# Kernel tuning notes

Hardware: AMD Instinct MI355X
Metric: run time of the kernel (lower is better)

Reference implementation:

```python
import jax, jax.numpy as jnp
import numpy as np

N_NODES = 100000
N_EDGES = 1600000
IN_CH = 128
HID = 64
N_CLASSES = 16
N_GRAPHS = 64


def setup_inputs() -> dict:
    key = jax.random.key(0)
    ks = jax.random.split(key, 10)
    x = jax.random.normal(ks[0], (N_NODES, IN_CH), dtype=jnp.float32)
    edge_index = jax.random.randint(ks[1], (2, N_EDGES), 0, N_NODES, dtype=jnp.int64)
    edge_weight = jax.random.uniform(ks[2], (N_EDGES,), dtype=jnp.float32)
    batch = jnp.sort(jax.random.randint(ks[3], (N_NODES,), 0, N_GRAPHS, dtype=jnp.int64))
    s1 = 1.0 / np.sqrt(IN_CH)
    s2 = 1.0 / np.sqrt(HID)
    W1 = jax.random.uniform(ks[4], (IN_CH, HID), jnp.float32, -s1, s1)
    b1 = jnp.zeros((HID,), jnp.float32)
    W2 = jax.random.uniform(ks[5], (HID, HID), jnp.float32, -s2, s2)
    b2 = jnp.zeros((HID,), jnp.float32)
    Wl = jax.random.uniform(ks[6], (HID, N_CLASSES), jnp.float32, -s2, s2)
    bl = jax.random.uniform(ks[7], (N_CLASSES,), jnp.float32, -s2, s2)
    return {"x": x, "edge_index": edge_index, "edge_weight": edge_weight,
            "batch": batch, "W1": W1, "b1": b1, "W2": W2, "b2": b2,
            "Wl": Wl, "bl": bl}


def _gcn_conv(x, src, dst, ew, W, b, n_nodes):
    # PyG GCNConv: h = x @ W; symmetric normalization with self-loops;
    # out[dst] += norm * h[src]; out += bias.
    deg = jax.ops.segment_sum(ew, dst, num_segments=n_nodes)
    deg_inv_sqrt = jnp.where(deg > 0, jax.lax.rsqrt(jnp.maximum(deg, 1e-30)), 0.0)
    norm = deg_inv_sqrt[src] * ew * deg_inv_sqrt[dst]  # [E']
    h = x @ W                                          # [N, out]
    msg = h[src] * norm[:, None]                       # [E', out] gather
    out = jax.ops.segment_sum(msg, dst, num_segments=n_nodes)  # scatter-add
    return out + b


def reference(x, edge_index, edge_weight, batch, W1, b1, W2, b2, Wl, bl):
    n = x.shape[0]
    # add self loops once (weight 1.0), shared by both conv layers
    loop = jnp.arange(n, dtype=edge_index.dtype)
    src = jnp.concatenate([edge_index[0], loop])
    dst = jnp.concatenate([edge_index[1], loop])
    ew = jnp.concatenate([edge_weight, jnp.ones((n,), edge_weight.dtype)])

    h = jax.nn.relu(_gcn_conv(x, src, dst, ew, W1, b1, n))
    h = jax.nn.relu(_gcn_conv(h, src, dst, ew, W2, b2, n))

    # global_mean_pool over graphs
    sums = jax.ops.segment_sum(h, batch, num_segments=N_GRAPHS)  # [G, HID]
    cnt = jax.ops.segment_sum(jnp.ones((n,), h.dtype), batch, num_segments=N_GRAPHS)
    pooled = sums / jnp.maximum(cnt, 1.0)[:, None]

    return pooled @ Wl + bl
```

## Files before the change

### kernel.cpp

```cpp
#include <hip/hip_runtime.h>
#include <hip/hip_fp16.h>

#define N_NODES   100000
#define N_EDGES   1600000
#define IN_CH     128
#define HID       64
#define N_CLASSES 16
#define N_GRAPHS  64

#define BK_SH     9
#define BK_NODES  512
#define NB        ((N_NODES + BK_NODES - 1) / BK_NODES)
#define BK_CAP    10240
#define CH_EDGES  4096
#define EPT       16
#define NCH       ((N_EDGES + CH_EDGES - 1) / CH_EDGES)

typedef __attribute__((ext_vector_type(8))) short bf16x8;
typedef __attribute__((ext_vector_type(4))) float f32x4;

__device__ __forceinline__ unsigned short f2bf(float f) {
    unsigned u = __float_as_uint(f);
    u += 0x7fffu + ((u >> 16) & 1u);
    return (unsigned short)(u >> 16);
}
__device__ __forceinline__ float4 bf4(uint2 v) {
    float4 o;
    o.x = __uint_as_float(v.x << 16);
    o.y = __uint_as_float(v.x & 0xffff0000u);
    o.z = __uint_as_float(v.y << 16);
    o.w = __uint_as_float(v.y & 0xffff0000u);
    return o;
}
__device__ __forceinline__ float dec_norm(unsigned v) {
    return __half2float(__ushort_as_half((unsigned short)(v >> 17)));
}

__global__ void k_init(int* __restrict__ bcursor, float* __restrict__ pooled,
                       float* __restrict__ cnt) {
    int i = blockIdx.x * 256 + threadIdx.x;
    if (i < NB) bcursor[i] = i * BK_CAP;
    if (i < N_GRAPHS * HID) pooled[i] = 0.0f;
    if (i < N_GRAPHS) cnt[i] = 0.0f;
}

__global__ void k_binscatter(const int* __restrict__ src, const int* __restrict__ dst,
                             const float* __restrict__ ew, int* __restrict__ bcursor,
                             int2* __restrict__ bedges) {
    __shared__ int  hist[NB];
    __shared__ int  offs[NB];
    __shared__ int  gbase[NB];
    __shared__ int  sc[256];
    __shared__ int2 stage[CH_EDGES];
    __shared__ int  dest[CH_EDGES];
    const int t = threadIdx.x;
    const int base = blockIdx.x * CH_EDGES;
    const int nloc = min(CH_EDGES, N_EDGES - base);

    for (int i = t; i < NB; i += 256) hist[i] = 0;
    __syncthreads();

    int myb[EPT], myr[EPT], myp[EPT]; float myw[EPT];
#pragma unroll
    for (int j = 0; j < EPT; ++j) {
        int i = base + j * 256 + t;
        if (i < N_EDGES) {
            int s = src[i], d = dst[i];
            int b = d >> BK_SH;
            myb[j] = b;
            myr[j] = atomicAdd(&hist[b], 1);
            myp[j] = s | ((d & (BK_NODES - 1)) << 17);
            myw[j] = ew[i];
        } else {
            myb[j] = -1;
        }
    }
    __syncthreads();

    int v = (t < NB) ? hist[t] : 0;
    sc[t] = v;
    __syncthreads();
    for (int off = 1; off < 256; off <<= 1) {
        int a = (t >= off) ? sc[t - off] : 0;
        __syncthreads();
        sc[t] += a;
        __syncthreads();
    }
    if (t < NB) {
        offs[t] = sc[t] - v;
        gbase[t] = (v > 0) ? atomicAdd(&bcursor[t], v) : 0;
    }
    __syncthreads();

#pragma unroll
    for (int j = 0; j < EPT; ++j) {
        if (myb[j] >= 0) {
            int p = offs[myb[j]] + myr[j];
            stage[p] = make_int2(myp[j], __float_as_int(myw[j]));
            dest[p] = gbase[myb[j]] + myr[j];
        }
    }
    __syncthreads();

    for (int i = t; i < nloc; i += 256)
        bedges[dest[i]] = stage[i];
}

__global__ void k_build1(const int* __restrict__ bcursor, const int2* __restrict__ bedges,
                         int2* __restrict__ rowse, float* __restrict__ dis) {
    __shared__ int   cnt[BK_NODES];
    __shared__ float dsum[BK_NODES];
    __shared__ int   sc[256];
    const int b = blockIdx.x;
    const int t = threadIdx.x;
    const int beg = b * BK_CAP, end = bcursor[b];

    for (int i = t; i < BK_NODES; i += 256) { cnt[i] = 0; dsum[i] = 0.0f; }
    __syncthreads();

    for (int i = beg + t; i < end; i += 256) {
        int2 e = bedges[i];
        int dl = ((unsigned)e.x) >> 17;
        atomicAdd(&cnt[dl], 1);
        atomicAdd(&dsum[dl], __int_as_float(e.y));
    }
    __syncthreads();

    int a0 = cnt[2 * t], a1 = cnt[2 * t + 1];
    int pair = a0 + a1;
    sc[t] = pair;
    __syncthreads();
    for (int off = 1; off < 256; off <<= 1) {
        int a = (t >= off) ? sc[t - off] : 0;
        __syncthreads();
        sc[t] += a;
        __syncthreads();
    }
    int excl = sc[t] - pair;
    {
        int n0 = b * BK_NODES + 2 * t;
        if (n0 < N_NODES) {
            rowse[n0] = make_int2(beg + excl, beg + excl + a0);
            dis[n0] = rsqrtf(1.0f + dsum[2 * t]);
        }
        int n1 = n0 + 1;
        if (n1 < N_NODES) {
            rowse[n1] = make_int2(beg + excl + a0, beg + excl + a0 + a1);
            dis[n1] = rsqrtf(1.0f + dsum[2 * t + 1]);
        }
    }
}

__global__ void k_build2(const int* __restrict__ bcursor, const int2* __restrict__ bedges,
                         const int2* __restrict__ rowse, const float* __restrict__ dis,
                         unsigned* __restrict__ csr) {
    __shared__ int   cur[BK_NODES];
    __shared__ float ldis[BK_NODES];
    const int b = blockIdx.x;
    const int t = threadIdx.x;
    const int beg = b * BK_CAP, end = bcursor[b];
    const int nb = b * BK_NODES;

    for (int i = t; i < BK_NODES; i += 256) {
        int nd = nb + i;
        cur[i]  = (nd < N_NODES) ? rowse[nd].x - beg : 0;
        ldis[i] = (nd < N_NODES) ? dis[nd] : 0.0f;
    }
    __syncthreads();

    for (int i = beg + t; i < end; i += 256) {
        int2 e = bedges[i];
        int dl = ((unsigned)e.x) >> 17;
        int s = e.x & 0x1FFFF;
        float nm = ldis[dl] * __int_as_float(e.y) * dis[s];
        unsigned short nb16 = __half_as_ushort(__float2half(nm)) & 0x7FFF;
        int pos = beg + atomicAdd(&cur[dl], 1);
        csr[pos] = (unsigned)s | ((unsigned)nb16 << 17);
    }
}

template <int K>
__global__ __launch_bounds__(256) void k_gemm(const float* __restrict__ x,
                                              const float* __restrict__ W,
                                              unsigned short* __restrict__ hb) {
    constexpr int AS = K + 8;
    __shared__ unsigned short a_s[64 * AS];
    __shared__ unsigned short wt[64 * AS];
    const int t    = threadIdx.x;
    const int lane = t & 63;
    const int wave = t >> 6;
    const int m    = lane & 15;
    const int quad = lane >> 4;
    const int rowbase = blockIdx.x * 64;

    constexpr int CPR = K / 8;
    for (int c = t; c < 64 * CPR; c += 256) {
        int row = c / CPR, cc = c % CPR;
        int gr = rowbase + row;
        float4 v0, v1;
        if (gr < N_NODES) {
            v0 = *(const float4*)&x[(long)gr * K + cc * 8];
            v1 = *(const float4*)&x[(long)gr * K + cc * 8 + 4];
        } else {
            v0 = make_float4(0.f, 0.f, 0.f, 0.f); v1 = v0;
        }
        uint4 p;
        p.x = f2bf(v0.x) | ((unsigned)f2bf(v0.y) << 16);
        p.y = f2bf(v0.z) | ((unsigned)f2bf(v0.w) << 16);
        p.z = f2bf(v1.x) | ((unsigned)f2bf(v1.y) << 16);
        p.w = f2bf(v1.z) | ((unsigned)f2bf(v1.w) << 16);
        *(uint4*)&a_s[row * AS + cc * 8] = p;
    }
    for (int idx = t; idx < K * 64; idx += 256) {
        int k = idx >> 6, n = idx & 63;
        wt[n * AS + k] = f2bf(W[idx]);
    }
    __syncthreads();

    bf16x8 bfrag[4][K / 32];
#pragma unroll
    for (int nt = 0; nt < 4; ++nt)
#pragma unroll
        for (int ks = 0; ks < K / 32; ++ks)
            bfrag[nt][ks] = *(const bf16x8*)&wt[(nt * 16 + m) * AS + ks * 32 + quad * 8];

    f32x4 acc[4];
#pragma unroll
    for (int nt = 0; nt < 4; ++nt) acc[nt] = (f32x4){0.f, 0.f, 0.f, 0.f};

#pragma unroll
    for (int ks = 0; ks < K / 32; ++ks) {
        bf16x8 af = *(const bf16x8*)&a_s[(wave * 16 + m) * AS + ks * 32 + quad * 8];
#pragma unroll
        for (int nt = 0; nt < 4; ++nt)
            acc[nt] = __builtin_amdgcn_mfma_f32_16x16x32_bf16(af, bfrag[nt][ks],
                                                              acc[nt], 0, 0, 0);
    }

#pragma unroll
    for (int nt = 0; nt < 4; ++nt) {
#pragma unroll
        for (int i = 0; i < 4; ++i) {
            int gr = rowbase + wave * 16 + quad * 4 + i;
            if (gr < N_NODES)
                hb[(long)gr * HID + nt * 16 + m] = f2bf(acc[nt][i]);
        }
    }
}

__global__ void k_aggregate(const int2* __restrict__ rowse, const unsigned* __restrict__ csr,
                            const uint2* __restrict__ hb, const float* __restrict__ dis,
                            const float* __restrict__ b, float4* __restrict__ out4) {
    const int tid  = threadIdx.x;
    const int lane = tid & 63;
    const int node = blockIdx.x * 4 + (tid >> 6);
    const int g    = lane >> 4;
    const int c4   = lane & 15;
    if (node >= N_NODES) return;

    const float d = dis[node];
    float4 hs = bf4(hb[node * 16 + c4]);
    float wself = (g == 0) ? d * d : 0.0f;
    float4 acc;
    acc.x = wself * hs.x; acc.y = wself * hs.y;
    acc.z = wself * hs.z; acc.w = wself * hs.w;

    const int2 rs = rowse[node];
    int p = rs.x;
    const int end = rs.y;

    unsigned d0, d1, d2, d3;
    if (p + 16 <= end) {
        d0 = csr[p + g];     d1 = csr[p + 4 + g];
        d2 = csr[p + 8 + g]; d3 = csr[p + 12 + g];
    }
    while (p + 16 <= end) {
        const unsigned e0 = d0, e1 = d1, e2 = d2, e3 = d3;
        const int pn = p + 16;
        if (pn + 16 <= end) {
            d0 = csr[pn + g];     d1 = csr[pn + 4 + g];
            d2 = csr[pn + 8 + g]; d3 = csr[pn + 12 + g];
        }
        float4 v0 = bf4(hb[(e0 & 0x1FFFF) * 16 + c4]);
        float4 v1 = bf4(hb[(e1 & 0x1FFFF) * 16 + c4]);
        float4 v2 = bf4(hb[(e2 & 0x1FFFF) * 16 + c4]);
        float4 v3 = bf4(hb[(e3 & 0x1FFFF) * 16 + c4]);
        float w0 = dec_norm(e0), w1 = dec_norm(e1);
        float w2 = dec_norm(e2), w3 = dec_norm(e3);
        acc.x += w0 * v0.x; acc.y += w0 * v0.y; acc.z += w0 * v0.z; acc.w += w0 * v0.w;
        acc.x += w1 * v1.x; acc.y += w1 * v1.y; acc.z += w1 * v1.z; acc.w += w1 * v1.w;
        acc.x += w2 * v2.x; acc.y += w2 * v2.y; acc.z += w2 * v2.z; acc.w += w2 * v2.w;
        acc.x += w3 * v3.x; acc.y += w3 * v3.y; acc.z += w3 * v3.z; acc.w += w3 * v3.w;
        p = pn;
    }
    if (p < end) {
        int i0 = p + g, i1 = p + 4 + g, i2 = p + 8 + g, i3 = p + 12 + g;
        unsigned e0 = csr[min(i0, end - 1)];
        unsigned e1 = csr[min(i1, end - 1)];
        unsigned e2 = csr[min(i2, end - 1)];
        unsigned e3 = csr[min(i3, end - 1)];
        float4 v0 = bf4(hb[(e0 & 0x1FFFF) * 16 + c4]);
        float4 v1 = bf4(hb[(e1 & 0x1FFFF) * 16 + c4]);
        float4 v2 = bf4(hb[(e2 & 0x1FFFF) * 16 + c4]);
        float4 v3 = bf4(hb[(e3 & 0x1FFFF) * 16 + c4]);
        float w0 = (i0 < end) ? dec_norm(e0) : 0.0f;
        float w1 = (i1 < end) ? dec_norm(e1) : 0.0f;
        float w2 = (i2 < end) ? dec_norm(e2) : 0.0f;
        float w3 = (i3 < end) ? dec_norm(e3) : 0.0f;
        acc.x += w0 * v0.x; acc.y += w0 * v0.y; acc.z += w0 * v0.z; acc.w += w0 * v0.w;
        acc.x += w1 * v1.x; acc.y += w1 * v1.y; acc.z += w1 * v1.z; acc.w += w1 * v1.w;
        acc.x += w2 * v2.x; acc.y += w2 * v2.y; acc.z += w2 * v2.z; acc.w += w2 * v2.w;
        acc.x += w3 * v3.x; acc.y += w3 * v3.y; acc.z += w3 * v3.z; acc.w += w3 * v3.w;
    }

    acc.x += __shfl_xor(acc.x, 16); acc.y += __shfl_xor(acc.y, 16);
    acc.z += __shfl_xor(acc.z, 16); acc.w += __shfl_xor(acc.w, 16);
    acc.x += __shfl_xor(acc.x, 32); acc.y += __shfl_xor(acc.y, 32);
    acc.z += __shfl_xor(acc.z, 32); acc.w += __shfl_xor(acc.w, 32);

    if (g == 0) {
        const float4 bb = ((const float4*)b)[c4];
        float4 o;
        o.x = fmaxf(acc.x + bb.x, 0.0f);
        o.y = fmaxf(acc.y + bb.y, 0.0f);
        o.z = fmaxf(acc.z + bb.z, 0.0f);
        o.w = fmaxf(acc.w + bb.w, 0.0f);
        out4[node * 16 + c4] = o;
    }
}

#define POOL_NPB 256
__global__ __launch_bounds__(1024) void k_pool(const float* __restrict__ agg,
                                               const int* __restrict__ batch,
                                               float* __restrict__ pooled,
                                               float* __restrict__ cnt) {
    __shared__ float psh[N_GRAPHS * HID];
    __shared__ float csh[N_GRAPHS];
    const int tid = threadIdx.x;
    const int c = tid & 63;
    const int w = tid >> 6;
    const int nodebase = blockIdx.x * POOL_NPB + w * 16;

    for (int i = tid; i < N_GRAPHS * HID; i += 1024) psh[i] = 0.f;
    if (tid < N_GRAPHS) csh[tid] = 0.f;
    __syncthreads();

    int curg = -1; float accv = 0.f, cntacc = 0.f;
    for (int j = 0; j < 16; ++j) {
        int node = nodebase + j;
        if (node >= N_NODES) break;
        int g = batch[node];
        float v = agg[node * HID + c];
        if (g != curg) {
            if (curg >= 0) {
                atomicAdd(&psh[curg * HID + c], accv);
                if (c == 0) atomicAdd(&csh[curg], cntacc);
            }
            curg = g; accv = 0.f; cntacc = 0.f;
        }
        accv += v; cntacc += 1.f;
    }
    if (curg >= 0) {
        atomicAdd(&psh[curg * HID + c], accv);
        if (c == 0) atomicAdd(&csh[curg], cntacc);
    }
    __syncthreads();

    for (int i = tid; i < N_GRAPHS * HID; i += 1024) {
        if (csh[i >> 6] > 0.f) atomicAdd(&pooled[i], psh[i]);
    }
    if (tid < N_GRAPHS && csh[tid] > 0.f) atomicAdd(&cnt[tid], csh[tid]);
}

__global__ void k_out(const float* __restrict__ pooled, const float* __restrict__ cnt,
                      const float* __restrict__ Wl, const float* __restrict__ bl,
                      float* __restrict__ out) {
    int tid = threadIdx.x;
    int g = tid >> 4, k = tid & 15;
    float inv = 1.0f / fmaxf(cnt[g], 1.0f);
    float acc = 0.f;
#pragma unroll
    for (int h = 0; h < HID; ++h) acc += pooled[g * HID + h] * Wl[h * N_CLASSES + k];
    out[g * N_CLASSES + k] = acc * inv + bl[k];
}

extern "C" void kernel_launch(void* const* d_in, const int* in_sizes, int n_in,
                              void* d_out, int out_size, void* d_ws, size_t ws_size,
                              hipStream_t stream) {
    const float* x     = (const float*)d_in[0];
    const int*   ei    = (const int*)d_in[1];
    const float* ew    = (const float*)d_in[2];
    const int*   batch = (const int*)d_in[3];
    const float* W1    = (const float*)d_in[4];
    const float* b1    = (const float*)d_in[5];
    const float* W2    = (const float*)d_in[6];
    const float* b2    = (const float*)d_in[7];
    const float* Wl    = (const float*)d_in[8];
    const float* bl    = (const float*)d_in[9];

    const int* srcv = ei;
    const int* dstv = ei + N_EDGES;

    char* wsb = (char*)d_ws;
    float*          dis    = (float*)wsb;              wsb += 100352 * 4;
    int2*           rowse  = (int2*)wsb;               wsb += 100352 * 8;
    int*            bcursor= (int*)wsb;                wsb += 256 * 4;
    unsigned*       csr    = (unsigned*)wsb;           wsb += (size_t)NB * BK_CAP * 4;
    unsigned short* hb     = (unsigned short*)wsb;     wsb += N_NODES * HID * 2;
    float*          agg    = (float*)wsb;              wsb += N_NODES * HID * 4;
    float*          pooled = (float*)wsb;              wsb += N_GRAPHS * HID * 4;
    float*          cnt    = (float*)wsb;              wsb += N_GRAPHS * 4;
    float*          out    = (float*)d_out;
    int2*           bedges = (int2*)agg;

    k_init<<<16, 256, 0, stream>>>(bcursor, pooled, cnt);
    k_binscatter<<<NCH, 256, 0, stream>>>(srcv, dstv, ew, bcursor, bedges);
    k_build1<<<NB, 256, 0, stream>>>(bcursor, bedges, rowse, dis);
    k_build2<<<NB, 256, 0, stream>>>(bcursor, bedges, rowse, dis, csr);

    k_gemm<IN_CH><<<(N_NODES + 63) / 64, 256, 0, stream>>>(x, W1, hb);
    k_aggregate<<<(N_NODES + 3) / 4, 256, 0, stream>>>(rowse, csr, (const uint2*)hb,
                                                       dis, b1, (float4*)agg);
    k_gemm<HID><<<(N_NODES + 63) / 64, 256, 0, stream>>>(agg, W2, hb);
    k_aggregate<<<(N_NODES + 3) / 4, 256, 0, stream>>>(rowse, csr, (const uint2*)hb,
                                                       dis, b2, (float4*)agg);

    k_pool<<<(N_NODES + POOL_NPB - 1) / POOL_NPB, 1024, 0, stream>>>(
        agg, batch, pooled, cnt);
    k_out<<<1, N_GRAPHS * N_CLASSES, 0, stream>>>(pooled, cnt, Wl, bl, out);
}
```

Baseline: 273.0 us.

## Factor symmetric normalization into GEMM epilogue and fuse CSR build passes

```diff
diff --git a/kernel.cpp b/kernel.cpp
--- a/kernel.cpp
+++ b/kernel.cpp
@@ -32,7 +32,7 @@
     o.w = __uint_as_float(v.y & 0xffff0000u);
     return o;
 }
-__device__ __forceinline__ float dec_norm(unsigned v) {
+__device__ __forceinline__ float dec_ew(unsigned v) {
     return __half2float(__ushort_as_half((unsigned short)(v >> 17)));
 }
 
@@ -106,20 +106,27 @@
         bedges[dest[i]] = stage[i];
 }
 
-__global__ void k_build1(const int* __restrict__ bcursor, const int2* __restrict__ bedges,
-                         int2* __restrict__ rowse, float* __restrict__ dis) {
+__global__ __launch_bounds__(256) void k_build(const int* __restrict__ bcursor,
+                                               const int2* __restrict__ bedges,
+                                               int2* __restrict__ rowse,
+                                               float* __restrict__ dis,
+                                               unsigned* __restrict__ csr) {
+    __shared__ int2  eds[BK_CAP];
     __shared__ int   cnt[BK_NODES];
     __shared__ float dsum[BK_NODES];
+    __shared__ int   cur[BK_NODES];
     __shared__ int   sc[256];
     const int b = blockIdx.x;
     const int t = threadIdx.x;
     const int beg = b * BK_CAP, end = bcursor[b];
+    const int n = end - beg;
 
     for (int i = t; i < BK_NODES; i += 256) { cnt[i] = 0; dsum[i] = 0.0f; }
     __syncthreads();
 
-    for (int i = beg + t; i < end; i += 256) {
-        int2 e = bedges[i];
+    for (int i = t; i < n; i += 256) {
+        int2 e = bedges[beg + i];
+        eds[i] = e;
         int dl = ((unsigned)e.x) >> 17;
         atomicAdd(&cnt[dl], 1);
         atomicAdd(&dsum[dl], __int_as_float(e.y));
@@ -137,6 +144,8 @@
         __syncthreads();
     }
     int excl = sc[t] - pair;
+    cur[2 * t] = excl;
+    cur[2 * t + 1] = excl + a0;
     {
         int n0 = b * BK_NODES + 2 * t;
         if (n0 < N_NODES) {
@@ -149,39 +158,22 @@
             dis[n1] = rsqrtf(1.0f + dsum[2 * t + 1]);
         }
     }
-}
-
-__global__ void k_build2(const int* __restrict__ bcursor, const int2* __restrict__ bedges,
-                         const int2* __restrict__ rowse, const float* __restrict__ dis,
-                         unsigned* __restrict__ csr) {
-    __shared__ int   cur[BK_NODES];
-    __shared__ float ldis[BK_NODES];
-    const int b = blockIdx.x;
-    const int t = threadIdx.x;
-    const int beg = b * BK_CAP, end = bcursor[b];
-    const int nb = b * BK_NODES;
-
-    for (int i = t; i < BK_NODES; i += 256) {
-        int nd = nb + i;
-        cur[i]  = (nd < N_NODES) ? rowse[nd].x - beg : 0;
-        ldis[i] = (nd < N_NODES) ? dis[nd] : 0.0f;
-    }
-    __syncthreads();
-
-    for (int i = beg + t; i < end; i += 256) {
-        int2 e = bedges[i];
+    __syncthreads();
+
+    for (int i = t; i < n; i += 256) {
+        int2 e = eds[i];
         int dl = ((unsigned)e.x) >> 17;
         int s = e.x & 0x1FFFF;
-        float nm = ldis[dl] * __int_as_float(e.y) * dis[s];
-        unsigned short nb16 = __half_as_ushort(__float2half(nm)) & 0x7FFF;
+        unsigned short w16 = __half_as_ushort(__float2half(__int_as_float(e.y)));
         int pos = beg + atomicAdd(&cur[dl], 1);
-        csr[pos] = (unsigned)s | ((unsigned)nb16 << 17);
+        csr[pos] = (unsigned)s | ((unsigned)w16 << 17);
     }
 }
 
 template <int K>
 __global__ __launch_bounds__(256) void k_gemm(const float* __restrict__ x,
                                               const float* __restrict__ W,
+                                              const float* __restrict__ dis,
                                               unsigned short* __restrict__ hb) {
     constexpr int AS = K + 8;
     __shared__ unsigned short a_s[64 * AS];
@@ -238,12 +230,13 @@
     }
 
 #pragma unroll
-    for (int nt = 0; nt < 4; ++nt) {
-#pragma unroll
-        for (int i = 0; i < 4; ++i) {
-            int gr = rowbase + wave * 16 + quad * 4 + i;
-            if (gr < N_NODES)
-                hb[(long)gr * HID + nt * 16 + m] = f2bf(acc[nt][i]);
+    for (int i = 0; i < 4; ++i) {
+        int gr = rowbase + wave * 16 + quad * 4 + i;
+        if (gr < N_NODES) {
+            float dsc = dis[gr];
+#pragma unroll
+            for (int nt = 0; nt < 4; ++nt)
+                hb[(long)gr * HID + nt * 16 + m] = f2bf(dsc * acc[nt][i]);
         }
     }
 }
@@ -258,12 +251,10 @@
     const int c4   = lane & 15;
     if (node >= N_NODES) return;
 
-    const float d = dis[node];
     float4 hs = bf4(hb[node * 16 + c4]);
-    float wself = (g == 0) ? d * d : 0.0f;
     float4 acc;
-    acc.x = wself * hs.x; acc.y = wself * hs.y;
-    acc.z = wself * hs.z; acc.w = wself * hs.w;
+    if (g == 0) { acc = hs; }
+    else        { acc.x = 0.f; acc.y = 0.f; acc.z = 0.f; acc.w = 0.f; }
 
     const int2 rs = rowse[node];
     int p = rs.x;
@@ -285,8 +276,8 @@
         float4 v1 = bf4(hb[(e1 & 0x1FFFF) * 16 + c4]);
         float4 v2 = bf4(hb[(e2 & 0x1FFFF) * 16 + c4]);
         float4 v3 = bf4(hb[(e3 & 0x1FFFF) * 16 + c4]);
-        float w0 = dec_norm(e0), w1 = dec_norm(e1);
-        float w2 = dec_norm(e2), w3 = dec_norm(e3);
+        float w0 = dec_ew(e0), w1 = dec_ew(e1);
+        float w2 = dec_ew(e2), w3 = dec_ew(e3);
         acc.x += w0 * v0.x; acc.y += w0 * v0.y; acc.z += w0 * v0.z; acc.w += w0 * v0.w;
         acc.x += w1 * v1.x; acc.y += w1 * v1.y; acc.z += w1 * v1.z; acc.w += w1 * v1.w;
         acc.x += w2 * v2.x; acc.y += w2 * v2.y; acc.z += w2 * v2.z; acc.w += w2 * v2.w;
@@ -303,10 +294,10 @@
         float4 v1 = bf4(hb[(e1 & 0x1FFFF) * 16 + c4]);
         float4 v2 = bf4(hb[(e2 & 0x1FFFF) * 16 + c4]);
         float4 v3 = bf4(hb[(e3 & 0x1FFFF) * 16 + c4]);
-        float w0 = (i0 < end) ? dec_norm(e0) : 0.0f;
-        float w1 = (i1 < end) ? dec_norm(e1) : 0.0f;
-        float w2 = (i2 < end) ? dec_norm(e2) : 0.0f;
-        float w3 = (i3 < end) ? dec_norm(e3) : 0.0f;
+        float w0 = (i0 < end) ? dec_ew(e0) : 0.0f;
+        float w1 = (i1 < end) ? dec_ew(e1) : 0.0f;
+        float w2 = (i2 < end) ? dec_ew(e2) : 0.0f;
+        float w3 = (i3 < end) ? dec_ew(e3) : 0.0f;
         acc.x += w0 * v0.x; acc.y += w0 * v0.y; acc.z += w0 * v0.z; acc.w += w0 * v0.w;
         acc.x += w1 * v1.x; acc.y += w1 * v1.y; acc.z += w1 * v1.z; acc.w += w1 * v1.w;
         acc.x += w2 * v2.x; acc.y += w2 * v2.y; acc.z += w2 * v2.z; acc.w += w2 * v2.w;
@@ -319,12 +310,13 @@
     acc.z += __shfl_xor(acc.z, 32); acc.w += __shfl_xor(acc.w, 32);
 
     if (g == 0) {
+        const float dd = dis[node];
         const float4 bb = ((const float4*)b)[c4];
         float4 o;
-        o.x = fmaxf(acc.x + bb.x, 0.0f);
-        o.y = fmaxf(acc.y + bb.y, 0.0f);
-        o.z = fmaxf(acc.z + bb.z, 0.0f);
-        o.w = fmaxf(acc.w + bb.w, 0.0f);
+        o.x = fmaxf(dd * acc.x + bb.x, 0.0f);
+        o.y = fmaxf(dd * acc.y + bb.y, 0.0f);
+        o.z = fmaxf(dd * acc.z + bb.z, 0.0f);
+        o.w = fmaxf(dd * acc.w + bb.w, 0.0f);
         out4[node * 16 + c4] = o;
     }
 }
@@ -415,13 +407,12 @@
 
     k_init<<<16, 256, 0, stream>>>(bcursor, pooled, cnt);
     k_binscatter<<<NCH, 256, 0, stream>>>(srcv, dstv, ew, bcursor, bedges);
-    k_build1<<<NB, 256, 0, stream>>>(bcursor, bedges, rowse, dis);
-    k_build2<<<NB, 256, 0, stream>>>(bcursor, bedges, rowse, dis, csr);
-
-    k_gemm<IN_CH><<<(N_NODES + 63) / 64, 256, 0, stream>>>(x, W1, hb);
+    k_build<<<NB, 256, 0, stream>>>(bcursor, bedges, rowse, dis, csr);
+
+    k_gemm<IN_CH><<<(N_NODES + 63) / 64, 256, 0, stream>>>(x, W1, dis, hb);
     k_aggregate<<<(N_NODES + 3) / 4, 256, 0, stream>>>(rowse, csr, (const uint2*)hb,
                                                        dis, b1, (float4*)agg);
-    k_gemm<HID><<<(N_NODES + 63) / 64, 256, 0, stream>>>(agg, W2, hb);
+    k_gemm<HID><<<(N_NODES + 63) / 64, 256, 0, stream>>>(agg, W2, dis, hb);
     k_aggregate<<<(N_NODES + 3) / 4, 256, 0, stream>>>(rowse, csr, (const uint2*)hb,
                                                        dis, b2, (float4*)agg);
 
```

New measurement: 271.5 us. About the same (-0.6%).
